# Optimization experiments

Measured on AMD Instinct MI355X. Metric: run time of the kernel, lower is better.

The kernel has to match this reference:

```python
import jax, jax.numpy as jnp
import numpy as np

THRESH = 0.7
MIN_KEPT = 100000


def setup_inputs() -> dict:
    key = jax.random.key(0)
    k1, k2 = jax.random.split(key)
    N, C, H, W = 4, 19, 512, 1024
    logits = jax.random.normal(k1, (N, C, H, W), dtype=jnp.float32)
    targets = jax.random.randint(k2, (N, H, W), 0, C, dtype=jnp.int64)
    return {"logits": logits, "targets": targets}


def reference(logits, targets):
    # log_softmax over class dim, then per-pixel NLL gather.  [N,C,H,W] -> [N,H,W]
    log_p = jax.nn.log_softmax(logits, axis=1)
    nll = -jnp.take_along_axis(log_p, targets[:, None, :, :], axis=1)[:, 0]
    loss_flat = nll.reshape(-1)

    valid = loss_flat > 0  # mirrors `loss_flat > 0` validity test in torch code
    n_valid = valid.sum()

    # Descending sort with invalid pixels pushed to the end (-inf).
    sorted_loss = jnp.sort(jnp.where(valid, loss_flat, -jnp.inf))[::-1]

    n_keep = jnp.maximum(jnp.int32(MIN_KEPT), (THRESH * n_valid).astype(jnp.int32))
    n_keep = jnp.minimum(n_keep, n_valid.astype(jnp.int32))
    thresh_val = sorted_loss[jnp.maximum(n_keep - 1, 0)]

    mask = loss_flat >= thresh_val
    kept_sum = jnp.sum(jnp.where(mask, loss_flat, jnp.float32(0)))
    kept_cnt = jnp.maximum(mask.sum(), 1).astype(loss_flat.dtype)
    ohem_mean = kept_sum / kept_cnt

    # If no valid pixels, torch returns loss_flat.mean()
    return jnp.where(n_valid > 0, ohem_mean, loss_flat.mean())
```

## Files before the change

kernel.cpp:

```cpp
#include <hip/hip_runtime.h>

#define NBATCH 4
#define NCLS   19
#define HW     524288
#define NPIX   (NBATCH * HW)
#define NQ     (NPIX / 4)

#define H0        0
#define H1        2048
#define CT_SUM    4096
#define CT_CNT    4098
#define CT_TICKET 4099
#define CTRL_U32  4104
#define LOSS_OFF  32768

__global__ void zero_ctrl_k(unsigned* __restrict__ ctrl) {
    int i = blockIdx.x * blockDim.x + threadIdx.x;
    if (i < CTRL_U32) ctrl[i] = 0u;
}

__global__ __launch_bounds__(256) void loss_hist_k(const float* __restrict__ logits,
                                                   const int* __restrict__ targets,
                                                   float* __restrict__ loss,
                                                   unsigned* __restrict__ hist0) {
    __shared__ unsigned sh[2048];
    for (int i = threadIdx.x; i < 2048; i += 256) sh[i] = 0u;
    __syncthreads();

    int tid = blockIdx.x * blockDim.x + threadIdx.x;
    int stride = gridDim.x * blockDim.x;
    for (int q = tid; q < NQ; q += stride) {
        int p   = q << 2;
        int n   = p >> 19;
        int pix = p & (HW - 1);
        const float4* base = reinterpret_cast<const float4*>(
            logits + (size_t)n * NCLS * HW + pix);
        int4 t4 = *reinterpret_cast<const int4*>(targets + p);

        float s0 = 0.f, s1 = 0.f, s2 = 0.f, s3 = 0.f;
        float g0 = 0.f, g1 = 0.f, g2 = 0.f, g3 = 0.f;
#pragma unroll
        for (int c = 0; c < NCLS; ++c) {
            float4 val = base[c * (HW / 4)];
            s0 += __expf(val.x); s1 += __expf(val.y);
            s2 += __expf(val.z); s3 += __expf(val.w);
            if (c == t4.x) g0 = val.x;
            if (c == t4.y) g1 = val.y;
            if (c == t4.z) g2 = val.z;
            if (c == t4.w) g3 = val.w;
        }
        float l0 = __logf(s0) - g0;
        float l1 = __logf(s1) - g1;
        float l2 = __logf(s2) - g2;
        float l3 = __logf(s3) - g3;
        *reinterpret_cast<float4*>(loss + p) = make_float4(l0, l1, l2, l3);

        if (l0 > 0.f) atomicAdd(&sh[__float_as_uint(l0) >> 21], 1u);
        if (l1 > 0.f) atomicAdd(&sh[__float_as_uint(l1) >> 21], 1u);
        if (l2 > 0.f) atomicAdd(&sh[__float_as_uint(l2) >> 21], 1u);
        if (l3 > 0.f) atomicAdd(&sh[__float_as_uint(l3) >> 21], 1u);
    }
    __syncthreads();
    for (int i = threadIdx.x; i < 2048; i += 256) {
        unsigned vv = sh[i];
        if (vv) atomicAdd(&hist0[i], vv);
    }
}

__device__ __forceinline__ void scan_hist(const unsigned* __restrict__ ghist,
                                          unsigned* sh_h, unsigned* sh_c,
                                          unsigned* bcast, unsigned k_in,
                                          bool derive_k) {
    int t = threadIdx.x;
    for (int i = t; i < 2048; i += 256) sh_h[i] = ghist[i];
    __syncthreads();
    unsigned s = 0;
#pragma unroll
    for (int j = 0; j < 8; ++j) s += sh_h[t * 8 + j];
    sh_c[t] = s;
    __syncthreads();
    if (t == 0) {
        unsigned k = k_in, flag = 0;
        unsigned total = 0;
        for (int i = 0; i < 256; ++i) total += sh_c[i];
        if (derive_k) {
            if (total == 0) { flag = 1u; k = 1u; }
            else {
                long long kk = (long long)(0.7f * (float)total);
                if (kk < 100000) kk = 100000;
                if (kk > (long long)total) kk = (long long)total;
                k = (unsigned)kk;
            }
        }
        unsigned run = 0; int chunk = -1;
        for (int i = 255; i >= 0; --i) {
            if (run + sh_c[i] >= k) { chunk = i; break; }
            run += sh_c[i];
        }
        unsigned sel = 0, rank = 1;
        if (chunk >= 0) {
            for (int b = chunk * 8 + 7; b >= chunk * 8; --b) {
                if (run + sh_h[b] >= k) { sel = (unsigned)b; rank = k - run; break; }
                run += sh_h[b];
            }
        }
        bcast[0] = sel; bcast[1] = rank; bcast[2] = flag; bcast[3] = total;
    }
    __syncthreads();
}

__global__ __launch_bounds__(256) void refine_k(const float4* __restrict__ loss4,
                                                unsigned* __restrict__ ctrl) {
    __shared__ unsigned h[2048];
    __shared__ unsigned c[256];
    __shared__ unsigned bcast[4];
    scan_hist(ctrl + H0, h, c, bcast, 0u, true);
    unsigned sel0 = bcast[0];
    if (bcast[2]) return;

    for (int i = threadIdx.x; i < 2048; i += 256) h[i] = 0u;
    __syncthreads();

    int tid = blockIdx.x * blockDim.x + threadIdx.x;
    int stride = gridDim.x * blockDim.x;
    for (int q = tid; q < NQ; q += stride) {
        float4 v = loss4[q];
#define PROC(X) do { float x_ = (X); if (x_ > 0.f) { unsigned u_ = __float_as_uint(x_); \
        if ((u_ >> 21) == sel0) atomicAdd(&h[(u_ >> 10) & 0x7FFu], 1u); } } while (0)
        PROC(v.x); PROC(v.y); PROC(v.z); PROC(v.w);
#undef PROC
    }
    __syncthreads();
    for (int i = threadIdx.x; i < 2048; i += 256) {
        unsigned vv = h[i];
        if (vv) atomicAdd(&ctrl[H1 + i], vv);
    }
}

__global__ __launch_bounds__(256) void final_k(const float4* __restrict__ loss4,
                                               unsigned* __restrict__ ctrl,
                                               float* __restrict__ out, int nblocks) {
    __shared__ unsigned h[2048];
    __shared__ unsigned c[256];
    __shared__ unsigned bcast[4];
    scan_hist(ctrl + H0, h, c, bcast, 0u, true);
    unsigned sel0 = bcast[0], rank1 = bcast[1], flag = bcast[2];
    __syncthreads();
    scan_hist(ctrl + H1, h, c, bcast, rank1, false);
    unsigned sel1 = bcast[0];
    float thresh = __uint_as_float((sel0 << 21) | (sel1 << 10));

    double lsum = 0.0; unsigned lcnt = 0;
    int tid = blockIdx.x * blockDim.x + threadIdx.x;
    int stride = gridDim.x * blockDim.x;
    for (int q = tid; q < NQ; q += stride) {
        float4 v = loss4[q];
        if (flag || v.x >= thresh) { lsum += (double)v.x; lcnt++; }
        if (flag || v.y >= thresh) { lsum += (double)v.y; lcnt++; }
        if (flag || v.z >= thresh) { lsum += (double)v.z; lcnt++; }
        if (flag || v.w >= thresh) { lsum += (double)v.w; lcnt++; }
    }
    __shared__ double sd[256];
    __shared__ unsigned sc[256];
    int t = threadIdx.x;
    sd[t] = lsum; sc[t] = lcnt;
    __syncthreads();
    for (int o = 128; o > 0; o >>= 1) {
        if (t < o) { sd[t] += sd[t + o]; sc[t] += sc[t + o]; }
        __syncthreads();
    }
    if (t == 0) {
        atomicAdd(reinterpret_cast<double*>(ctrl + CT_SUM), sd[0]);
        atomicAdd(&ctrl[CT_CNT], sc[0]);
        __threadfence();
        unsigned tick = atomicAdd(&ctrl[CT_TICKET], 1u);
        if (tick == (unsigned)(nblocks - 1)) {
            double ssum = atomicAdd(reinterpret_cast<double*>(ctrl + CT_SUM), 0.0);
            unsigned cc = atomicAdd(&ctrl[CT_CNT], 0u);
            if (cc < 1u) cc = 1u;
            out[0] = (float)(ssum / (double)cc);
        }
    }
}

extern "C" void kernel_launch(void* const* d_in, const int* in_sizes, int n_in,
                              void* d_out, int out_size, void* d_ws, size_t ws_size,
                              hipStream_t stream) {
    const float* logits  = (const float*)d_in[0];
    const int*   targets = (const int*)d_in[1];
    float* out = (float*)d_out;
    unsigned* ctrl = (unsigned*)d_ws;
    float* loss = (float*)((char*)d_ws + LOSS_OFF);
    const float4* loss4 = (const float4*)loss;

    zero_ctrl_k<<<(CTRL_U32 + 255) / 256, 256, 0, stream>>>(ctrl);
    loss_hist_k<<<2048, 256, 0, stream>>>(logits, targets, loss, ctrl + H0);
    refine_k<<<1024, 256, 0, stream>>>(loss4, ctrl);
    final_k<<<1024, 256, 0, stream>>>(loss4, ctrl, out, 1024);
}
```

Measured before the change: 136.0 us.

## Fuse refine and final passes with grid barrier, replicate global histograms

Merges the refine and final kernels into one persistent kernel of 512 blocks that uses an atomic spin grid barrier between the second histogram pass and the masked sum. This removes a kernel launch and its drain. Global histograms are split into 8 copies to spread atomic contention, the zeroing kernel becomes a memset, and the loss kernel drops to 512 blocks. The grid barrier only works if all 512 blocks are resident at once, which launch_bounds(256,2) is meant to ensure, otherwise it deadlocks.

After: 125.3 us. 7.9% less time.

```diff
diff --git a/kernel.cpp b/kernel.cpp
--- a/kernel.cpp
+++ b/kernel.cpp
@@ -6,30 +6,32 @@
 #define NPIX   (NBATCH * HW)
 #define NQ     (NPIX / 4)
 
+#define NCOPY   8
+#define NBINS   2048
 #define H0        0
-#define H1        2048
-#define CT_SUM    4096
-#define CT_CNT    4098
-#define CT_TICKET 4099
-#define CTRL_U32  4104
-#define LOSS_OFF  32768
-
-__global__ void zero_ctrl_k(unsigned* __restrict__ ctrl) {
-    int i = blockIdx.x * blockDim.x + threadIdx.x;
-    if (i < CTRL_U32) ctrl[i] = 0u;
-}
+#define H1        (NCOPY * NBINS)
+#define CT_BASE   (2 * NCOPY * NBINS)
+#define CT_SUM    CT_BASE
+#define CT_CNT    (CT_BASE + 2)
+#define CT_TICKET (CT_BASE + 3)
+#define CT_BAR    (CT_BASE + 4)
+#define CTRL_U32  (CT_BASE + 8)
+#define LOSS_OFF  262144
+
+#define LH_BLOCKS 512
+#define FU_BLOCKS 512
 
 __global__ __launch_bounds__(256) void loss_hist_k(const float* __restrict__ logits,
                                                    const int* __restrict__ targets,
                                                    float* __restrict__ loss,
                                                    unsigned* __restrict__ hist0) {
-    __shared__ unsigned sh[2048];
-    for (int i = threadIdx.x; i < 2048; i += 256) sh[i] = 0u;
-    __syncthreads();
-
-    int tid = blockIdx.x * blockDim.x + threadIdx.x;
-    int stride = gridDim.x * blockDim.x;
-    for (int q = tid; q < NQ; q += stride) {
+    __shared__ unsigned sh[NBINS];
+    for (int i = threadIdx.x; i < NBINS; i += 256) sh[i] = 0u;
+    __syncthreads();
+
+    int tid = blockIdx.x * 256 + threadIdx.x;
+#pragma unroll 1
+    for (int q = tid; q < NQ; q += LH_BLOCKS * 256) {
         int p   = q << 2;
         int n   = p >> 19;
         int pix = p & (HW - 1);
@@ -61,9 +63,10 @@
         if (l3 > 0.f) atomicAdd(&sh[__float_as_uint(l3) >> 21], 1u);
     }
     __syncthreads();
-    for (int i = threadIdx.x; i < 2048; i += 256) {
+    unsigned* g = hist0 + (blockIdx.x & (NCOPY - 1)) * NBINS;
+    for (int i = threadIdx.x; i < NBINS; i += 256) {
         unsigned vv = sh[i];
-        if (vv) atomicAdd(&hist0[i], vv);
+        if (vv) atomicAdd(&g[i], vv);
     }
 }
 
@@ -72,7 +75,12 @@
                                           unsigned* bcast, unsigned k_in,
                                           bool derive_k) {
     int t = threadIdx.x;
-    for (int i = t; i < 2048; i += 256) sh_h[i] = ghist[i];
+    for (int i = t; i < NBINS; i += 256) {
+        unsigned s = 0;
+#pragma unroll
+        for (int k = 0; k < NCOPY; ++k) s += ghist[k * NBINS + i];
+        sh_h[i] = s;
+    }
     __syncthreads();
     unsigned s = 0;
 #pragma unroll
@@ -109,56 +117,63 @@
     __syncthreads();
 }
 
-__global__ __launch_bounds__(256) void refine_k(const float4* __restrict__ loss4,
-                                                unsigned* __restrict__ ctrl) {
-    __shared__ unsigned h[2048];
-    __shared__ unsigned c[256];
+__global__ __launch_bounds__(256, 2) void fused_k(const float4* __restrict__ loss4,
+                                                  unsigned* __restrict__ ctrl,
+                                                  float* __restrict__ out) {
+    __shared__ unsigned h[NBINS];
+    __shared__ unsigned c2[256];
     __shared__ unsigned bcast[4];
-    scan_hist(ctrl + H0, h, c, bcast, 0u, true);
-    unsigned sel0 = bcast[0];
-    if (bcast[2]) return;
-
-    for (int i = threadIdx.x; i < 2048; i += 256) h[i] = 0u;
-    __syncthreads();
-
-    int tid = blockIdx.x * blockDim.x + threadIdx.x;
-    int stride = gridDim.x * blockDim.x;
-    for (int q = tid; q < NQ; q += stride) {
+
+    scan_hist(ctrl + H0, h, c2, bcast, 0u, true);
+    unsigned sel0 = bcast[0], rank1 = bcast[1], flag = bcast[2];
+    __syncthreads();
+
+    int tid = blockIdx.x * 256 + threadIdx.x;
+    if (!flag) {
+        for (int i = threadIdx.x; i < NBINS; i += 256) h[i] = 0u;
+        __syncthreads();
+#pragma unroll 1
+        for (int q = tid; q < NQ; q += FU_BLOCKS * 256) {
+            float4 v = loss4[q];
+#define PROC(X) do { float x_ = (X); if (x_ > 0.f) { unsigned u_ = __float_as_uint(x_); \
+            if ((u_ >> 21) == sel0) atomicAdd(&h[(u_ >> 10) & 0x7FFu], 1u); } } while (0)
+            PROC(v.x); PROC(v.y); PROC(v.z); PROC(v.w);
+#undef PROC
+        }
+        __syncthreads();
+        unsigned* g = ctrl + H1 + (blockIdx.x & (NCOPY - 1)) * NBINS;
+        for (int i = threadIdx.x; i < NBINS; i += 256) {
+            unsigned vv = h[i];
+            if (vv) atomicAdd(&g[i], vv);
+        }
+    }
+
+    __syncthreads();
+    if (threadIdx.x == 0) {
+        __hip_atomic_fetch_add(&ctrl[CT_BAR], 1u, __ATOMIC_ACQ_REL, __HIP_MEMORY_SCOPE_AGENT);
+        while (__hip_atomic_load(&ctrl[CT_BAR], __ATOMIC_ACQUIRE, __HIP_MEMORY_SCOPE_AGENT)
+               < (unsigned)FU_BLOCKS) {
+            __builtin_amdgcn_s_sleep(2);
+        }
+    }
+    __syncthreads();
+
+    float thresh;
+    if (flag) {
+        thresh = -__builtin_inff();
+    } else {
+        scan_hist(ctrl + H1, h, c2, bcast, rank1, false);
+        thresh = __uint_as_float((sel0 << 21) | (bcast[0] << 10));
+    }
+
+    double lsum = 0.0; unsigned lcnt = 0;
+#pragma unroll 1
+    for (int q = tid; q < NQ; q += FU_BLOCKS * 256) {
         float4 v = loss4[q];
-#define PROC(X) do { float x_ = (X); if (x_ > 0.f) { unsigned u_ = __float_as_uint(x_); \
-        if ((u_ >> 21) == sel0) atomicAdd(&h[(u_ >> 10) & 0x7FFu], 1u); } } while (0)
-        PROC(v.x); PROC(v.y); PROC(v.z); PROC(v.w);
-#undef PROC
-    }
-    __syncthreads();
-    for (int i = threadIdx.x; i < 2048; i += 256) {
-        unsigned vv = h[i];
-        if (vv) atomicAdd(&ctrl[H1 + i], vv);
-    }
-}
-
-__global__ __launch_bounds__(256) void final_k(const float4* __restrict__ loss4,
-                                               unsigned* __restrict__ ctrl,
-                                               float* __restrict__ out, int nblocks) {
-    __shared__ unsigned h[2048];
-    __shared__ unsigned c[256];
-    __shared__ unsigned bcast[4];
-    scan_hist(ctrl + H0, h, c, bcast, 0u, true);
-    unsigned sel0 = bcast[0], rank1 = bcast[1], flag = bcast[2];
-    __syncthreads();
-    scan_hist(ctrl + H1, h, c, bcast, rank1, false);
-    unsigned sel1 = bcast[0];
-    float thresh = __uint_as_float((sel0 << 21) | (sel1 << 10));
-
-    double lsum = 0.0; unsigned lcnt = 0;
-    int tid = blockIdx.x * blockDim.x + threadIdx.x;
-    int stride = gridDim.x * blockDim.x;
-    for (int q = tid; q < NQ; q += stride) {
-        float4 v = loss4[q];
-        if (flag || v.x >= thresh) { lsum += (double)v.x; lcnt++; }
-        if (flag || v.y >= thresh) { lsum += (double)v.y; lcnt++; }
-        if (flag || v.z >= thresh) { lsum += (double)v.z; lcnt++; }
-        if (flag || v.w >= thresh) { lsum += (double)v.w; lcnt++; }
+        if (v.x >= thresh) { lsum += (double)v.x; lcnt++; }
+        if (v.y >= thresh) { lsum += (double)v.y; lcnt++; }
+        if (v.z >= thresh) { lsum += (double)v.z; lcnt++; }
+        if (v.w >= thresh) { lsum += (double)v.w; lcnt++; }
     }
     __shared__ double sd[256];
     __shared__ unsigned sc[256];
@@ -174,7 +189,7 @@
         atomicAdd(&ctrl[CT_CNT], sc[0]);
         __threadfence();
         unsigned tick = atomicAdd(&ctrl[CT_TICKET], 1u);
-        if (tick == (unsigned)(nblocks - 1)) {
+        if (tick == (unsigned)(FU_BLOCKS - 1)) {
             double ssum = atomicAdd(reinterpret_cast<double*>(ctrl + CT_SUM), 0.0);
             unsigned cc = atomicAdd(&ctrl[CT_CNT], 0u);
             if (cc < 1u) cc = 1u;
@@ -193,8 +208,7 @@
     float* loss = (float*)((char*)d_ws + LOSS_OFF);
     const float4* loss4 = (const float4*)loss;
 
-    zero_ctrl_k<<<(CTRL_U32 + 255) / 256, 256, 0, stream>>>(ctrl);
-    loss_hist_k<<<2048, 256, 0, stream>>>(logits, targets, loss, ctrl + H0);
-    refine_k<<<1024, 256, 0, stream>>>(loss4, ctrl);
-    final_k<<<1024, 256, 0, stream>>>(loss4, ctrl, out, 1024);
-}
+    hipMemsetAsync(ctrl, 0, CTRL_U32 * sizeof(unsigned), stream);
+    loss_hist_k<<<LH_BLOCKS, 256, 0, stream>>>(logits, targets, loss, ctrl + H0);
+    fused_k<<<FU_BLOCKS, 256, 0, stream>>>(loss4, ctrl, out);
+}
```
